# Kernel optimization log

Measured on AMD Instinct MI355X. Metric: run time of the kernel, lower is better.

The kernel has to match this reference:

```python
import jax, jax.numpy as jnp
import numpy as np

EPS = 1e-8  # torch.nn.CosineSimilarity default eps


def setup_inputs() -> dict:
    key = jax.random.key(0)
    batch = jax.random.normal(key, (8192, 128), dtype=jnp.float32)
    return {"batch": batch}


def reference(batch):
    B = batch.shape[0]
    # Full pairwise cosine similarity matrix S[i, j]
    norms = jnp.linalg.norm(batch, axis=1)                      # [B]
    denom = jnp.maximum(norms[:, None] * norms[None, :], EPS)   # [B, B]
    S = (batch @ batch.T) / denom                                # [B, B]
    # Denominator of soft_nll(i, j): sum_{m != i} exp(S[i, m])
    expS = jnp.exp(S)
    Z = expS.sum(axis=1) - jnp.diagonal(expS)                    # [B]
    logZ = jnp.log(Z)                                            # [B]
    # term(i, j) = -log( exp(S[i,j]) / Z_i ) = -S[i,j] + logZ_i
    # Original loop: for k in 1..(B+1)//2 - 1, pairs (2k-1, 2k) 1-indexed
    N = (B + 1) // 2
    ks = jnp.arange(1, N)
    i = 2 * ks - 2  # 0-indexed first element of pair
    j = 2 * ks - 1  # 0-indexed second element of pair
    pair_loss = (-S[i, j] + logZ[i]) + (-S[j, i] + logZ[j])
    return jnp.sum(pair_loss) / B
```

## Files before the change

### kernel.cpp

```cpp
#include <hip/hip_runtime.h>
#include <hip/hip_bf16.h>

typedef __attribute__((ext_vector_type(8))) short short8;
typedef __attribute__((ext_vector_type(4))) float floatx4;

#define B_ROWS 8192
#define DIM 128
#define NPAIR 4095
#define RSCALE 1.2011224087864498f

#define GLOAD_LDS16(gp, lp)                                                     \
    __builtin_amdgcn_global_load_lds(                                           \
        (const __attribute__((address_space(1))) void*)(gp),                    \
        (__attribute__((address_space(3))) void*)(lp), 16, 0, 0)

__global__ void kzero(float* __restrict__ Z) {
    int i = blockIdx.x * 256 + threadIdx.x;
    if (i < B_ROWS) Z[i] = 0.f;
}

__global__ void kprep(const float* __restrict__ X, __hip_bfloat16* __restrict__ XN,
                      float* __restrict__ pairT, float* __restrict__ out) {
    __shared__ float2 lds[4][64];
    const int wid = threadIdx.x >> 6;
    const int lane = threadIdx.x & 63;
    const int row = blockIdx.x * 4 + wid;

    const float2 v = *reinterpret_cast<const float2*>(X + row * DIM + lane * 2);
    float ss = v.x * v.x + v.y * v.y;
    #pragma unroll
    for (int m = 1; m < 64; m <<= 1) ss += __shfl_xor(ss, m, 64);
    const float rn = ss > 0.f ? rsqrtf(ss) : 0.f;
    const float2 nv = make_float2(v.x * rn, v.y * rn);

    *reinterpret_cast<__hip_bfloat162*>(XN + row * DIM + lane * 2) =
        __float22bfloat162_rn(make_float2(nv.x * RSCALE, nv.y * RSCALE));
    lds[wid][lane] = nv;
    __syncthreads();

    if ((wid & 1) == 0) {
        const int p = blockIdx.x * 2 + (wid >> 1);
        if (p < NPAIR) {
            const float2 a = lds[wid][lane];
            const float2 b = lds[wid + 1][lane];
            float d = a.x * b.x + a.y * b.y;
            #pragma unroll
            for (int m = 1; m < 64; m <<= 1) d += __shfl_xor(d, m, 64);
            if (lane == 0) pairT[p] = d;
        }
    }
    if (blockIdx.x == 0 && threadIdx.x == 0) out[0] = 0.f;
}

__device__ __forceinline__ void stage_half(const __hip_bfloat16* __restrict__ gsrc,
                                           __hip_bfloat16* lbuf, int tid) {
    const int wid = tid >> 6;
    const int lane = tid & 63;
    #pragma unroll
    for (int it = 0; it < 4; ++it) {
        const int woff = it * 2048 + wid * 512;
        const int e = woff + lane * 8;
        const int src = (e & ~127) | ((e & 127) ^ (((e >> 7) & 7) << 3));
        GLOAD_LDS16(gsrc + src, lbuf + woff);
    }
}

template <bool USEP>
__global__ void __launch_bounds__(256, 2) kgemm(const __hip_bfloat16* __restrict__ XN,
                                                float* __restrict__ ZP) {
    __shared__ __hip_bfloat16 Bs[3][64 * DIM];

    const int tid = threadIdx.x;
    const int wid = tid >> 6;
    const int lane = tid & 63;
    const int lr = lane & 15;
    const int lk = lane >> 4;
    const int wr = wid >> 1;
    const int wc = wid & 1;
    const int rb = blockIdx.y;
    const int g = blockIdx.x;

    short8 a[4][4];
    const __hip_bfloat16* Abase = XN + (rb * 128 + wr * 64 + lr) * DIM + lk * 8;
    #pragma unroll
    for (int m = 0; m < 4; ++m)
        #pragma unroll
        for (int kk = 0; kk < 4; ++kk)
            a[kk][m] = *reinterpret_cast<const short8*>(Abase + m * 16 * DIM + kk * 32);

    float rp[4][4];
    #pragma unroll
    for (int m = 0; m < 4; ++m)
        #pragma unroll
        for (int r = 0; r < 4; ++r) rp[m][r] = 0.f;

    const floatx4 zero4 = {0.f, 0.f, 0.f, 0.f};

    stage_half(XN + (size_t)(g * 8) * 128 * DIM, Bs[0], tid);
    stage_half(XN + ((size_t)(g * 8) * 128 + 64) * DIM, Bs[1], tid);

    for (int t = 0; t < 16; ++t) {
        if (t < 15)
            asm volatile("s_waitcnt vmcnt(4)" ::: "memory");
        else
            asm volatile("s_waitcnt vmcnt(0)" ::: "memory");
        __builtin_amdgcn_s_barrier();

        if (t + 2 < 16)
            stage_half(XN + ((size_t)(g * 8 + ((t + 2) >> 1)) * 128 + ((t + 2) & 1) * 64) * DIM,
                       Bs[(t + 2) % 3], tid);

        const __hip_bfloat16* Bt = Bs[t % 3];
        const int cbj = g * 8 + (t >> 1);
        const bool dzero = (cbj == rb) && ((t & 1) == wr);

        __builtin_amdgcn_s_setprio(1);
        short8 b[4][2];
        #pragma unroll
        for (int n = 0; n < 2; ++n) {
            const int row = wc * 32 + n * 16 + lr;
            #pragma unroll
            for (int kk = 0; kk < 4; ++kk) {
                const int col = (kk * 32 + lk * 8) ^ ((row & 7) << 3);
                b[kk][n] = *reinterpret_cast<const short8*>(&Bt[row * DIM + col]);
            }
        }

        floatx4 acc[4][2];
        #pragma unroll
        for (int m = 0; m < 4; ++m)
            #pragma unroll
            for (int n = 0; n < 2; ++n)
                acc[m][n] = __builtin_amdgcn_mfma_f32_16x16x32_bf16(a[0][m], b[0][n], zero4, 0, 0, 0);
        #pragma unroll
        for (int kk = 1; kk < 4; ++kk)
            #pragma unroll
            for (int m = 0; m < 4; ++m)
                #pragma unroll
                for (int n = 0; n < 2; ++n)
                    acc[m][n] = __builtin_amdgcn_mfma_f32_16x16x32_bf16(a[kk][m], b[kk][n], acc[m][n], 0, 0, 0);
        __builtin_amdgcn_s_setprio(0);

        if (dzero) {
            #pragma unroll
            for (int m = 0; m < 4; ++m)
                #pragma unroll
                for (int n = 0; n < 2; ++n)
                    #pragma unroll
                    for (int r = 0; r < 4; ++r) {
                        float e = __builtin_amdgcn_exp2f(acc[m][n][r]);
                        if (m * 16 + lk * 4 + r == wc * 32 + n * 16 + lr) e = 0.f;
                        rp[m][r] += e;
                    }
        } else {
            #pragma unroll
            for (int m = 0; m < 4; ++m)
                #pragma unroll
                for (int n = 0; n < 2; ++n)
                    #pragma unroll
                    for (int r = 0; r < 4; ++r)
                        rp[m][r] += __builtin_amdgcn_exp2f(acc[m][n][r]);
        }
    }

    #pragma unroll
    for (int m = 0; m < 4; ++m)
        #pragma unroll
        for (int r = 0; r < 4; ++r) {
            float v = rp[m][r];
            v += __shfl_xor(v, 1, 64);
            v += __shfl_xor(v, 2, 64);
            v += __shfl_xor(v, 4, 64);
            v += __shfl_xor(v, 8, 64);
            if (lr == 0) {
                const int row = rb * 128 + wr * 64 + m * 16 + lk * 4 + r;
                if (USEP)
                    ZP[(g * 2 + wc) * B_ROWS + row] = v;
                else
                    atomicAdd(&ZP[row], v);
            }
        }
}

__global__ void kfinalP(const float* __restrict__ P, const float* __restrict__ pairT,
                        float* __restrict__ out) {
    const int r = blockIdx.x * 256 + threadIdx.x;
    float s = 0.f;
    if (r < B_ROWS - 2) {
        float z = 0.f;
        #pragma unroll
        for (int tt = 0; tt < 16; ++tt) z += P[tt * B_ROWS + r];
        s = logf(z);
    }
    if (r < NPAIR) s -= 2.f * pairT[r];
    #pragma unroll
    for (int m = 1; m < 64; m <<= 1) s += __shfl_xor(s, m, 64);
    __shared__ float red[4];
    const int wid = threadIdx.x >> 6;
    const int lane = threadIdx.x & 63;
    if (lane == 0) red[wid] = s;
    __syncthreads();
    if (threadIdx.x == 0) {
        float tsum = red[0] + red[1] + red[2] + red[3];
        atomicAdd(out, tsum / (float)B_ROWS);
    }
}

__global__ void kfinalZ(const float* __restrict__ Z, const float* __restrict__ pairT,
                        float* __restrict__ out) {
    float s = 0.f;
    for (int r = threadIdx.x; r < B_ROWS - 2; r += 1024) s += logf(Z[r]);
    for (int p = threadIdx.x; p < NPAIR; p += 1024) s -= 2.f * pairT[p];
    #pragma unroll
    for (int m = 1; m < 64; m <<= 1) s += __shfl_xor(s, m, 64);
    __shared__ float red[16];
    const int wid = threadIdx.x >> 6;
    const int lane = threadIdx.x & 63;
    if (lane == 0) red[wid] = s;
    __syncthreads();
    if (threadIdx.x == 0) {
        float t = 0.f;
        #pragma unroll
        for (int i = 0; i < 16; ++i) t += red[i];
        out[0] = t / (float)B_ROWS;
    }
}

extern "C" void kernel_launch(void* const* d_in, const int* in_sizes, int n_in,
                              void* d_out, int out_size, void* d_ws, size_t ws_size,
                              hipStream_t stream) {
    (void)in_sizes; (void)n_in; (void)out_size;
    const float* X = (const float*)d_in[0];
    float* out = (float*)d_out;
    char* ws = (char*)d_ws;

    float* Z = (float*)ws;
    float* pairT = (float*)(ws + 32768);
    __hip_bfloat16* XN = (__hip_bfloat16*)(ws + 49152);
    float* P = (float*)(ws + 49152 + 2097152);
    const size_t need = 49152 + 2097152 + (size_t)16 * B_ROWS * 4;
    const bool useP = ws_size >= need;

    kprep<<<2048, 256, 0, stream>>>(X, XN, pairT, out);
    if (useP) {
        kgemm<true><<<dim3(8, 64), 256, 0, stream>>>(XN, P);
        kfinalP<<<32, 256, 0, stream>>>(P, pairT, out);
    } else {
        kzero<<<32, 256, 0, stream>>>(Z);
        kgemm<false><<<dim3(8, 64), 256, 0, stream>>>(XN, Z);
        kfinalZ<<<1, 1024, 0, stream>>>(Z, pairT, out);
    }
}
```

Measured before the change: 34.05 us.

## Software-pipeline GEMM tiles with ping-pong accumulators overlapping exp and MFMA

Restructures the tile loop into two alternating phases with double-buffered B fragments and accumulators. The B fragments for the next tile are read from LDS ahead of use, and the exp/row-sum of the previous tile runs after the current tile's MFMAs are issued, so exp and LDS latency can hide behind matrix work. In exchange it waits for all outstanding global loads (vmcnt(0)) every phase instead of vmcnt(4), drops the s_setprio hints, and roughly doubles accumulator and fragment register use, which could raise register pressure.

```diff
diff --git a/kernel.cpp b/kernel.cpp
--- a/kernel.cpp
+++ b/kernel.cpp
@@ -65,6 +65,75 @@
     }
 }
 
+#define LOADB(BN, BUF)                                                          \
+    {                                                                           \
+        const __hip_bfloat16* Bn_ = (BUF);                                      \
+        _Pragma("unroll")                                                       \
+        for (int n_ = 0; n_ < 2; ++n_) {                                        \
+            const int row_ = wc * 32 + n_ * 16 + lr;                            \
+            _Pragma("unroll")                                                   \
+            for (int kk_ = 0; kk_ < 4; ++kk_) {                                 \
+                const int col_ = (kk_ * 32 + lk * 8) ^ ((row_ & 7) << 3);       \
+                BN[kk_][n_] =                                                   \
+                    *reinterpret_cast<const short8*>(&Bn_[row_ * DIM + col_]);  \
+            }                                                                   \
+        }                                                                       \
+    }
+
+#define EXPACC(AP, TE)                                                          \
+    {                                                                           \
+        const int cbj_ = g * 8 + ((TE) >> 1);                                   \
+        const bool dz_ = (cbj_ == rb) && (((TE) & 1) == wr);                    \
+        if (dz_) {                                                              \
+            _Pragma("unroll")                                                   \
+            for (int m_ = 0; m_ < 4; ++m_)                                      \
+                _Pragma("unroll")                                               \
+                for (int n_ = 0; n_ < 2; ++n_)                                  \
+                    _Pragma("unroll")                                           \
+                    for (int r_ = 0; r_ < 4; ++r_) {                            \
+                        float e_ = __builtin_amdgcn_exp2f(AP[m_][n_][r_]);      \
+                        if (m_ * 16 + lk * 4 + r_ == wc * 32 + n_ * 16 + lr)    \
+                            e_ = 0.f;                                           \
+                        rp[m_][r_] += e_;                                       \
+                    }                                                           \
+        } else {                                                                \
+            _Pragma("unroll")                                                   \
+            for (int m_ = 0; m_ < 4; ++m_)                                      \
+                _Pragma("unroll")                                               \
+                for (int n_ = 0; n_ < 2; ++n_)                                  \
+                    _Pragma("unroll")                                           \
+                    for (int r_ = 0; r_ < 4; ++r_)                              \
+                        rp[m_][r_] += __builtin_amdgcn_exp2f(AP[m_][n_][r_]);   \
+        }                                                                       \
+    }
+
+#define PHASE(AC, AP, BC, BN, T, DOEXP)                                         \
+    {                                                                           \
+        asm volatile("s_waitcnt vmcnt(0)" ::: "memory");                        \
+        __builtin_amdgcn_s_barrier();                                           \
+        __builtin_amdgcn_sched_barrier(0);                                      \
+        if ((T) + 2 < 16)                                                       \
+            stage_half(XN + ((size_t)(g * 8 + (((T) + 2) >> 1)) * 128 +         \
+                             (((T) + 2) & 1) * 64) * DIM,                       \
+                       Bs[((T) + 2) % 3], tid);                                 \
+        if ((T) + 1 < 16) LOADB(BN, Bs[((T) + 1) % 3]);                         \
+        _Pragma("unroll")                                                       \
+        for (int m_ = 0; m_ < 4; ++m_)                                          \
+            _Pragma("unroll")                                                   \
+            for (int n_ = 0; n_ < 2; ++n_)                                      \
+                AC[m_][n_] = __builtin_amdgcn_mfma_f32_16x16x32_bf16(           \
+                    a[0][m_], BC[0][n_], zero4, 0, 0, 0);                       \
+        _Pragma("unroll")                                                       \
+        for (int kk_ = 1; kk_ < 4; ++kk_)                                       \
+            _Pragma("unroll")                                                   \
+            for (int m_ = 0; m_ < 4; ++m_)                                      \
+                _Pragma("unroll")                                               \
+                for (int n_ = 0; n_ < 2; ++n_)                                  \
+                    AC[m_][n_] = __builtin_amdgcn_mfma_f32_16x16x32_bf16(       \
+                        a[kk_][m_], BC[kk_][n_], AC[m_][n_], 0, 0, 0);          \
+        if (DOEXP) EXPACC(AP, (T) - 1);                                         \
+    }
+
 template <bool USEP>
 __global__ void __launch_bounds__(256, 2) kgemm(const __hip_bfloat16* __restrict__ XN,
                                                 float* __restrict__ ZP) {
@@ -95,73 +164,21 @@
         for (int r = 0; r < 4; ++r) rp[m][r] = 0.f;
 
     const floatx4 zero4 = {0.f, 0.f, 0.f, 0.f};
+    short8 bA[4][2], bB[4][2];
+    floatx4 accA[4][2], accB[4][2];
 
     stage_half(XN + (size_t)(g * 8) * 128 * DIM, Bs[0], tid);
     stage_half(XN + ((size_t)(g * 8) * 128 + 64) * DIM, Bs[1], tid);
-
-    for (int t = 0; t < 16; ++t) {
-        if (t < 15)
-            asm volatile("s_waitcnt vmcnt(4)" ::: "memory");
-        else
-            asm volatile("s_waitcnt vmcnt(0)" ::: "memory");
-        __builtin_amdgcn_s_barrier();
-
-        if (t + 2 < 16)
-            stage_half(XN + ((size_t)(g * 8 + ((t + 2) >> 1)) * 128 + ((t + 2) & 1) * 64) * DIM,
-                       Bs[(t + 2) % 3], tid);
-
-        const __hip_bfloat16* Bt = Bs[t % 3];
-        const int cbj = g * 8 + (t >> 1);
-        const bool dzero = (cbj == rb) && ((t & 1) == wr);
-
-        __builtin_amdgcn_s_setprio(1);
-        short8 b[4][2];
-        #pragma unroll
-        for (int n = 0; n < 2; ++n) {
-            const int row = wc * 32 + n * 16 + lr;
-            #pragma unroll
-            for (int kk = 0; kk < 4; ++kk) {
-                const int col = (kk * 32 + lk * 8) ^ ((row & 7) << 3);
-                b[kk][n] = *reinterpret_cast<const short8*>(&Bt[row * DIM + col]);
-            }
-        }
-
-        floatx4 acc[4][2];
-        #pragma unroll
-        for (int m = 0; m < 4; ++m)
-            #pragma unroll
-            for (int n = 0; n < 2; ++n)
-                acc[m][n] = __builtin_amdgcn_mfma_f32_16x16x32_bf16(a[0][m], b[0][n], zero4, 0, 0, 0);
-        #pragma unroll
-        for (int kk = 1; kk < 4; ++kk)
-            #pragma unroll
-            for (int m = 0; m < 4; ++m)
-                #pragma unroll
-                for (int n = 0; n < 2; ++n)
-                    acc[m][n] = __builtin_amdgcn_mfma_f32_16x16x32_bf16(a[kk][m], b[kk][n], acc[m][n], 0, 0, 0);
-        __builtin_amdgcn_s_setprio(0);
-
-        if (dzero) {
-            #pragma unroll
-            for (int m = 0; m < 4; ++m)
-                #pragma unroll
-                for (int n = 0; n < 2; ++n)
-                    #pragma unroll
-                    for (int r = 0; r < 4; ++r) {
-                        float e = __builtin_amdgcn_exp2f(acc[m][n][r]);
-                        if (m * 16 + lk * 4 + r == wc * 32 + n * 16 + lr) e = 0.f;
-                        rp[m][r] += e;
-                    }
-        } else {
-            #pragma unroll
-            for (int m = 0; m < 4; ++m)
-                #pragma unroll
-                for (int n = 0; n < 2; ++n)
-                    #pragma unroll
-                    for (int r = 0; r < 4; ++r)
-                        rp[m][r] += __builtin_amdgcn_exp2f(acc[m][n][r]);
-        }
-    }
+    asm volatile("s_waitcnt vmcnt(4)" ::: "memory");
+    __builtin_amdgcn_s_barrier();
+    __builtin_amdgcn_sched_barrier(0);
+    LOADB(bA, Bs[0]);
+
+    for (int t = 0; t < 16; t += 2) {
+        PHASE(accA, accB, bA, bB, t, (t > 0));
+        PHASE(accB, accA, bB, bA, t + 1, true);
+    }
+    EXPACC(accB, 15);
 
     #pragma unroll
     for (int m = 0; m < 4; ++m)
```

After: 33.99 us. Within noise of the previous version (-0.2%).

## Fuse final reduction into GEMM via last-block counter and widen prep loads

Applied to the files above, without the earlier changes.

Drops the separate final-reduction kernel. Each GEMM block writes its partial row sums to a row-major P buffer, then increments a per-row-block counter. The last of the 8 column blocks for a row block reads P, computes the log terms and pair terms, and atomically adds to the output. kprep now handles two rows per wavefront with float4 loads and computes pair dots via cross-half shuffles with no LDS or barrier. The launch grid becomes 1D with rb as the fast index. This saves a kernel launch and the P re-read pass, at the cost of a threadfence, counter atomics, a nondeterministic float atomic sum order, and removing the ws_size check.

```diff
diff --git a/kernel.cpp b/kernel.cpp
--- a/kernel.cpp
+++ b/kernel.cpp
@@ -14,42 +14,42 @@
         (const __attribute__((address_space(1))) void*)(gp),                    \
         (__attribute__((address_space(3))) void*)(lp), 16, 0, 0)
 
-__global__ void kzero(float* __restrict__ Z) {
-    int i = blockIdx.x * 256 + threadIdx.x;
-    if (i < B_ROWS) Z[i] = 0.f;
-}
-
 __global__ void kprep(const float* __restrict__ X, __hip_bfloat16* __restrict__ XN,
-                      float* __restrict__ pairT, float* __restrict__ out) {
-    __shared__ float2 lds[4][64];
+                      float* __restrict__ pairT, float* __restrict__ out,
+                      int* __restrict__ cnt) {
     const int wid = threadIdx.x >> 6;
     const int lane = threadIdx.x & 63;
-    const int row = blockIdx.x * 4 + wid;
-
-    const float2 v = *reinterpret_cast<const float2*>(X + row * DIM + lane * 2);
-    float ss = v.x * v.x + v.y * v.y;
-    #pragma unroll
-    for (int m = 1; m < 64; m <<= 1) ss += __shfl_xor(ss, m, 64);
+    const int j = lane & 31;
+    const int W = blockIdx.x * 4 + wid;
+    const int row = 2 * W + (lane >> 5);
+
+    const float4 v = *reinterpret_cast<const float4*>(X + row * DIM + j * 4);
+    float ss = v.x * v.x + v.y * v.y + v.z * v.z + v.w * v.w;
+    #pragma unroll
+    for (int m = 1; m < 32; m <<= 1) ss += __shfl_xor(ss, m, 64);
     const float rn = ss > 0.f ? rsqrtf(ss) : 0.f;
-    const float2 nv = make_float2(v.x * rn, v.y * rn);
-
-    *reinterpret_cast<__hip_bfloat162*>(XN + row * DIM + lane * 2) =
-        __float22bfloat162_rn(make_float2(nv.x * RSCALE, nv.y * RSCALE));
-    lds[wid][lane] = nv;
-    __syncthreads();
-
-    if ((wid & 1) == 0) {
-        const int p = blockIdx.x * 2 + (wid >> 1);
-        if (p < NPAIR) {
-            const float2 a = lds[wid][lane];
-            const float2 b = lds[wid + 1][lane];
-            float d = a.x * b.x + a.y * b.y;
-            #pragma unroll
-            for (int m = 1; m < 64; m <<= 1) d += __shfl_xor(d, m, 64);
-            if (lane == 0) pairT[p] = d;
-        }
-    }
-    if (blockIdx.x == 0 && threadIdx.x == 0) out[0] = 0.f;
+
+    float4 pv;
+    pv.x = __shfl_xor(v.x, 32, 64);
+    pv.y = __shfl_xor(v.y, 32, 64);
+    pv.z = __shfl_xor(v.z, 32, 64);
+    pv.w = __shfl_xor(v.w, 32, 64);
+    float pd = v.x * pv.x + v.y * pv.y + v.z * pv.z + v.w * pv.w;
+    #pragma unroll
+    for (int m = 1; m < 32; m <<= 1) pd += __shfl_xor(pd, m, 64);
+    const float rno = __shfl_xor(rn, 32, 64);
+    if (lane == 0 && W < NPAIR) pairT[W] = pd * rn * rno;
+
+    const float sc = rn * RSCALE;
+    __hip_bfloat162 h0 = __float22bfloat162_rn(make_float2(v.x * sc, v.y * sc));
+    __hip_bfloat162 h1 = __float22bfloat162_rn(make_float2(v.z * sc, v.w * sc));
+    struct B4 { __hip_bfloat162 a, b; };
+    *reinterpret_cast<B4*>(XN + row * DIM + j * 4) = B4{h0, h1};
+
+    if (blockIdx.x == 0) {
+        if (threadIdx.x == 0) out[0] = 0.f;
+        if (threadIdx.x < 64) cnt[threadIdx.x] = 0;
+    }
 }
 
 __device__ __forceinline__ void stage_half(const __hip_bfloat16* __restrict__ gsrc,
@@ -65,9 +65,11 @@
     }
 }
 
-template <bool USEP>
 __global__ void __launch_bounds__(256, 2) kgemm(const __hip_bfloat16* __restrict__ XN,
-                                                float* __restrict__ ZP) {
+                                                float* __restrict__ P,
+                                                const float* __restrict__ pairT,
+                                                float* __restrict__ out,
+                                                int* __restrict__ cnt) {
     __shared__ __hip_bfloat16 Bs[3][64 * DIM];
 
     const int tid = threadIdx.x;
@@ -77,8 +79,9 @@
     const int lk = lane >> 4;
     const int wr = wid >> 1;
     const int wc = wid & 1;
-    const int rb = blockIdx.y;
-    const int g = blockIdx.x;
+    const int id = blockIdx.x;
+    const int rb = id & 63;
+    const int g = id >> 6;
 
     short8 a[4][4];
     const __hip_bfloat16* Abase = XN + (rb * 128 + wr * 64 + lr) * DIM + lk * 8;
@@ -111,8 +114,7 @@
                        Bs[(t + 2) % 3], tid);
 
         const __hip_bfloat16* Bt = Bs[t % 3];
-        const int cbj = g * 8 + (t >> 1);
-        const bool dzero = (cbj == rb) && ((t & 1) == wr);
+        const bool dzero = (g * 8 + (t >> 1) == rb) && ((t & 1) == wr);
 
         __builtin_amdgcn_s_setprio(1);
         short8 b[4][2];
@@ -174,80 +176,55 @@
             v += __shfl_xor(v, 8, 64);
             if (lr == 0) {
                 const int row = rb * 128 + wr * 64 + m * 16 + lk * 4 + r;
-                if (USEP)
-                    ZP[(g * 2 + wc) * B_ROWS + row] = v;
-                else
-                    atomicAdd(&ZP[row], v);
+                P[row * 16 + (g * 2 + wc)] = v;
             }
         }
-}
-
-__global__ void kfinalP(const float* __restrict__ P, const float* __restrict__ pairT,
-                        float* __restrict__ out) {
-    const int r = blockIdx.x * 256 + threadIdx.x;
-    float s = 0.f;
-    if (r < B_ROWS - 2) {
-        float z = 0.f;
-        #pragma unroll
-        for (int tt = 0; tt < 16; ++tt) z += P[tt * B_ROWS + r];
-        s = logf(z);
-    }
-    if (r < NPAIR) s -= 2.f * pairT[r];
-    #pragma unroll
-    for (int m = 1; m < 64; m <<= 1) s += __shfl_xor(s, m, 64);
-    __shared__ float red[4];
-    const int wid = threadIdx.x >> 6;
-    const int lane = threadIdx.x & 63;
-    if (lane == 0) red[wid] = s;
+
+    __threadfence();
     __syncthreads();
-    if (threadIdx.x == 0) {
-        float tsum = red[0] + red[1] + red[2] + red[3];
-        atomicAdd(out, tsum / (float)B_ROWS);
-    }
-}
-
-__global__ void kfinalZ(const float* __restrict__ Z, const float* __restrict__ pairT,
-                        float* __restrict__ out) {
-    float s = 0.f;
-    for (int r = threadIdx.x; r < B_ROWS - 2; r += 1024) s += logf(Z[r]);
-    for (int p = threadIdx.x; p < NPAIR; p += 1024) s -= 2.f * pairT[p];
-    #pragma unroll
-    for (int m = 1; m < 64; m <<= 1) s += __shfl_xor(s, m, 64);
-    __shared__ float red[16];
-    const int wid = threadIdx.x >> 6;
-    const int lane = threadIdx.x & 63;
-    if (lane == 0) red[wid] = s;
-    __syncthreads();
-    if (threadIdx.x == 0) {
-        float t = 0.f;
-        #pragma unroll
-        for (int i = 0; i < 16; ++i) t += red[i];
-        out[0] = t / (float)B_ROWS;
+    if (wid == 0) {
+        int done = 0;
+        if (lane == 0) done = (atomicAdd(&cnt[rb], 1) == 7) ? 1 : 0;
+        done = __shfl(done, 0, 64);
+        if (done) {
+            __threadfence();
+            float s = 0.f;
+            #pragma unroll
+            for (int rr = 0; rr < 2; ++rr) {
+                const int row = rb * 128 + lane * 2 + rr;
+                if (row < B_ROWS - 2) {
+                    const float4* p4 = reinterpret_cast<const float4*>(P + row * 16);
+                    float z = 0.f;
+                    #pragma unroll
+                    for (int i = 0; i < 4; ++i) {
+                        const float4 vv = p4[i];
+                        z += vv.x + vv.y + vv.z + vv.w;
+                    }
+                    s += logf(z);
+                }
+            }
+            const int p = rb * 64 + lane;
+            if (p < NPAIR) s -= 2.f * pairT[p];
+            #pragma unroll
+            for (int m = 1; m < 64; m <<= 1) s += __shfl_xor(s, m, 64);
+            if (lane == 0) atomicAdd(out, s / (float)B_ROWS);
+        }
     }
 }
 
 extern "C" void kernel_launch(void* const* d_in, const int* in_sizes, int n_in,
                               void* d_out, int out_size, void* d_ws, size_t ws_size,
                               hipStream_t stream) {
-    (void)in_sizes; (void)n_in; (void)out_size;
+    (void)in_sizes; (void)n_in; (void)out_size; (void)ws_size;
     const float* X = (const float*)d_in[0];
     float* out = (float*)d_out;
     char* ws = (char*)d_ws;
 
-    float* Z = (float*)ws;
-    float* pairT = (float*)(ws + 32768);
-    __hip_bfloat16* XN = (__hip_bfloat16*)(ws + 49152);
-    float* P = (float*)(ws + 49152 + 2097152);
-    const size_t need = 49152 + 2097152 + (size_t)16 * B_ROWS * 4;
-    const bool useP = ws_size >= need;
-
-    kprep<<<2048, 256, 0, stream>>>(X, XN, pairT, out);
-    if (useP) {
-        kgemm<true><<<dim3(8, 64), 256, 0, stream>>>(XN, P);
-        kfinalP<<<32, 256, 0, stream>>>(P, pairT, out);
-    } else {
-        kzero<<<32, 256, 0, stream>>>(Z);
-        kgemm<false><<<dim3(8, 64), 256, 0, stream>>>(XN, Z);
-        kfinalZ<<<1, 1024, 0, stream>>>(Z, pairT, out);
-    }
-}
+    int* cnt = (int*)ws;
+    float* pairT = (float*)(ws + 4096);
+    __hip_bfloat16* XN = (__hip_bfloat16*)(ws + 32768);
+    float* P = (float*)(ws + 32768 + 2097152);
+
+    kprep<<<1024, 256, 0, stream>>>(X, XN, pairT, out, cnt);
+    kgemm<<<512, 256, 0, stream>>>(XN, P, pairT, out, cnt);
+}
```

Result: slower. 81.69 us (+139.9%).

## Double GEMM column split, transpose partial sums, and streamline prep kernel

Applied to the files above, without the earlier changes.

The GEMM grid now splits the columns into 16 groups of 512 instead of 8 groups of 1024, so each block runs 8 tile steps instead of 16. This doubles the block count to improve CU occupancy and tail balance, and launch bounds are raised to 3 blocks per CU. Partial row sums are stored row-major, 32 per row, so the final kernel reads them with contiguous float4 loads. The prep kernel now handles two rows per wave with float4 loads and computes pair dot products by shuffles instead of through LDS. In exchange, more A-fragment loads are repeated across the extra blocks, the partial buffer doubles in size, and the tighter launch bound may cause register spills.

```diff
diff --git a/kernel.cpp b/kernel.cpp
--- a/kernel.cpp
+++ b/kernel.cpp
@@ -21,35 +21,36 @@
 
 __global__ void kprep(const float* __restrict__ X, __hip_bfloat16* __restrict__ XN,
                       float* __restrict__ pairT, float* __restrict__ out) {
-    __shared__ float2 lds[4][64];
     const int wid = threadIdx.x >> 6;
     const int lane = threadIdx.x & 63;
-    const int row = blockIdx.x * 4 + wid;
-
-    const float2 v = *reinterpret_cast<const float2*>(X + row * DIM + lane * 2);
-    float ss = v.x * v.x + v.y * v.y;
-    #pragma unroll
-    for (int m = 1; m < 64; m <<= 1) ss += __shfl_xor(ss, m, 64);
+    const int j = lane & 31;
+    const int W = blockIdx.x * 4 + wid;
+    const int row = 2 * W + (lane >> 5);
+
+    const float4 v = *reinterpret_cast<const float4*>(X + row * DIM + j * 4);
+    float ss = v.x * v.x + v.y * v.y + v.z * v.z + v.w * v.w;
+    #pragma unroll
+    for (int m = 1; m < 32; m <<= 1) ss += __shfl_xor(ss, m, 64);
     const float rn = ss > 0.f ? rsqrtf(ss) : 0.f;
-    const float2 nv = make_float2(v.x * rn, v.y * rn);
-
-    *reinterpret_cast<__hip_bfloat162*>(XN + row * DIM + lane * 2) =
-        __float22bfloat162_rn(make_float2(nv.x * RSCALE, nv.y * RSCALE));
-    lds[wid][lane] = nv;
-    __syncthreads();
-
-    if ((wid & 1) == 0) {
-        const int p = blockIdx.x * 2 + (wid >> 1);
-        if (p < NPAIR) {
-            const float2 a = lds[wid][lane];
-            const float2 b = lds[wid + 1][lane];
-            float d = a.x * b.x + a.y * b.y;
-            #pragma unroll
-            for (int m = 1; m < 64; m <<= 1) d += __shfl_xor(d, m, 64);
-            if (lane == 0) pairT[p] = d;
-        }
-    }
-    if (blockIdx.x == 0 && threadIdx.x == 0) out[0] = 0.f;
+
+    float4 pv;
+    pv.x = __shfl_xor(v.x, 32, 64);
+    pv.y = __shfl_xor(v.y, 32, 64);
+    pv.z = __shfl_xor(v.z, 32, 64);
+    pv.w = __shfl_xor(v.w, 32, 64);
+    float pd = v.x * pv.x + v.y * pv.y + v.z * pv.z + v.w * pv.w;
+    #pragma unroll
+    for (int m = 1; m < 32; m <<= 1) pd += __shfl_xor(pd, m, 64);
+    const float rno = __shfl_xor(rn, 32, 64);
+    if (lane == 0 && W < NPAIR) pairT[W] = pd * rn * rno;
+
+    const float sc = rn * RSCALE;
+    __hip_bfloat162 h0 = __float22bfloat162_rn(make_float2(v.x * sc, v.y * sc));
+    __hip_bfloat162 h1 = __float22bfloat162_rn(make_float2(v.z * sc, v.w * sc));
+    struct B4 { __hip_bfloat162 a, b; };
+    *reinterpret_cast<B4*>(XN + row * DIM + j * 4) = B4{h0, h1};
+
+    if (W == 0 && lane == 0) out[0] = 0.f;
 }
 
 __device__ __forceinline__ void stage_half(const __hip_bfloat16* __restrict__ gsrc,
@@ -66,7 +67,7 @@
 }
 
 template <bool USEP>
-__global__ void __launch_bounds__(256, 2) kgemm(const __hip_bfloat16* __restrict__ XN,
+__global__ void __launch_bounds__(256, 3) kgemm(const __hip_bfloat16* __restrict__ XN,
                                                 float* __restrict__ ZP) {
     __shared__ __hip_bfloat16 Bs[3][64 * DIM];
 
@@ -96,23 +97,23 @@
 
     const floatx4 zero4 = {0.f, 0.f, 0.f, 0.f};
 
-    stage_half(XN + (size_t)(g * 8) * 128 * DIM, Bs[0], tid);
-    stage_half(XN + ((size_t)(g * 8) * 128 + 64) * DIM, Bs[1], tid);
-
-    for (int t = 0; t < 16; ++t) {
-        if (t < 15)
+    stage_half(XN + (size_t)(g * 512) * DIM, Bs[0], tid);
+    stage_half(XN + (size_t)(g * 512 + 64) * DIM, Bs[1], tid);
+
+    const int myblk = rb * 2 + wr;
+
+    for (int t = 0; t < 8; ++t) {
+        if (t < 7)
             asm volatile("s_waitcnt vmcnt(4)" ::: "memory");
         else
             asm volatile("s_waitcnt vmcnt(0)" ::: "memory");
         __builtin_amdgcn_s_barrier();
 
-        if (t + 2 < 16)
-            stage_half(XN + ((size_t)(g * 8 + ((t + 2) >> 1)) * 128 + ((t + 2) & 1) * 64) * DIM,
-                       Bs[(t + 2) % 3], tid);
+        if (t + 2 < 8)
+            stage_half(XN + (size_t)(g * 512 + (t + 2) * 64) * DIM, Bs[(t + 2) % 3], tid);
 
         const __hip_bfloat16* Bt = Bs[t % 3];
-        const int cbj = g * 8 + (t >> 1);
-        const bool dzero = (cbj == rb) && ((t & 1) == wr);
+        const bool dzero = (g * 8 + t == myblk);
 
         __builtin_amdgcn_s_setprio(1);
         short8 b[4][2];
@@ -175,7 +176,7 @@
             if (lr == 0) {
                 const int row = rb * 128 + wr * 64 + m * 16 + lk * 4 + r;
                 if (USEP)
-                    ZP[(g * 2 + wc) * B_ROWS + row] = v;
+                    ZP[row * 32 + (g * 2 + wc)] = v;
                 else
                     atomicAdd(&ZP[row], v);
             }
@@ -187,9 +188,13 @@
     const int r = blockIdx.x * 256 + threadIdx.x;
     float s = 0.f;
     if (r < B_ROWS - 2) {
+        const float4* p4 = reinterpret_cast<const float4*>(P + r * 32);
         float z = 0.f;
         #pragma unroll
-        for (int tt = 0; tt < 16; ++tt) z += P[tt * B_ROWS + r];
+        for (int i = 0; i < 8; ++i) {
+            const float4 v = p4[i];
+            z += v.x + v.y + v.z + v.w;
+        }
         s = logf(z);
     }
     if (r < NPAIR) s -= 2.f * pairT[r];
@@ -238,16 +243,16 @@
     float* pairT = (float*)(ws + 32768);
     __hip_bfloat16* XN = (__hip_bfloat16*)(ws + 49152);
     float* P = (float*)(ws + 49152 + 2097152);
-    const size_t need = 49152 + 2097152 + (size_t)16 * B_ROWS * 4;
+    const size_t need = 49152 + 2097152 + (size_t)32 * B_ROWS * 4;
     const bool useP = ws_size >= need;
 
-    kprep<<<2048, 256, 0, stream>>>(X, XN, pairT, out);
+    kprep<<<1024, 256, 0, stream>>>(X, XN, pairT, out);
     if (useP) {
-        kgemm<true><<<dim3(8, 64), 256, 0, stream>>>(XN, P);
+        kgemm<true><<<dim3(16, 64), 256, 0, stream>>>(XN, P);
         kfinalP<<<32, 256, 0, stream>>>(P, pairT, out);
     } else {
         kzero<<<32, 256, 0, stream>>>(Z);
-        kgemm<false><<<dim3(8, 64), 256, 0, stream>>>(XN, Z);
+        kgemm<false><<<dim3(16, 64), 256, 0, stream>>>(XN, Z);
         kfinalZ<<<1, 1024, 0, stream>>>(Z, pairT, out);
     }
 }
```

After: 37.38 us. +9.8%, slower.
